# Optimization experiments

Hardware: AMD Instinct MI355X
Metric: run time of the kernel (lower is better)

Reference implementation:

```python
import jax, jax.numpy as jnp
import numpy as np

S, D_IN, D, H, FF = 8192, 128, 2, 2, 3
EPS = 1e-5


def _ln(x, s, b):
    m = jnp.mean(x, axis=-1, keepdims=True)
    v = jnp.mean((x - m) ** 2, axis=-1, keepdims=True)
    return (x - m) / jnp.sqrt(v + EPS) * s + b


def _mha(q_in, kv_in, qkv_w, qkv_b, out_w, out_b):
    # torch nn.MultiheadAttention: packed in_proj weight [3D, D], post-scale 1/sqrt(dh)
    wq, wk, wv = jnp.split(qkv_w, 3, axis=0)
    bq, bk, bv = jnp.split(qkv_b, 3)
    dh = D // H
    heads = lambda t: t.reshape(-1, H, dh).transpose(1, 0, 2)  # [H, S, dh]
    q = heads(q_in @ wq.T + bq)
    k = heads(kv_in @ wk.T + bk)
    v = heads(kv_in @ wv.T + bv)
    scores = jnp.einsum('hqd,hkd->hqk', q, k) / jnp.sqrt(jnp.asarray(dh, q.dtype))
    a = jax.nn.softmax(scores, axis=-1)
    o = jnp.einsum('hqk,hkd->hqd', a, v).transpose(1, 0, 2).reshape(-1, D)
    return o @ out_w.T + out_b


def _ffn(x, w1, b1, w2, b2):
    return jax.nn.relu(x @ w1.T + b1) @ w2.T + b2


def _forward(x, rand_mask, inn_w, inn_b, enc_qkv_w, enc_qkv_b, enc_out_w, enc_out_b, enc_ln1_s, enc_ln1_b, enc_ln2_s, enc_ln2_b, enc_ff1_w, enc_ff1_b, enc_ff2_w, enc_ff2_b, enc_norm_s, enc_norm_b, dec_sa_qkv_w, dec_sa_qkv_b, dec_sa_out_w, dec_sa_out_b, dec_ca_qkv_w, dec_ca_qkv_b, dec_ca_out_w, dec_ca_out_b, dec_ln1_s, dec_ln1_b, dec_ln2_s, dec_ln2_b, dec_ln3_s, dec_ln3_b, dec_ff1_w, dec_ff1_b, dec_ff2_w, dec_ff2_b, dec_norm_s, dec_norm_b, out_w, out_b):
    # x * rand(S,128) -> Linear(128,2) -> ReLU  (dropout disabled: eval mode)
    h = jax.nn.relu((x * rand_mask) @ inn_w.T + inn_b)  # [S, 2]
    # ---- encoder (2 post-norm layers) + final LayerNorm ----
    src = h
    for i in range(2):
        src = _ln(src + _mha(src, src, enc_qkv_w[i], enc_qkv_b[i], enc_out_w[i], enc_out_b[i]), enc_ln1_s[i], enc_ln1_b[i])
        src = _ln(src + _ffn(src, enc_ff1_w[i], enc_ff1_b[i], enc_ff2_w[i], enc_ff2_b[i]), enc_ln2_s[i], enc_ln2_b[i])
    mem = _ln(src, enc_norm_s, enc_norm_b)
    # ---- decoder (1 post-norm layer, tgt = h, no masks) + final LayerNorm ----
    t = h
    t = _ln(t + _mha(t, t, dec_sa_qkv_w, dec_sa_qkv_b, dec_sa_out_w, dec_sa_out_b), dec_ln1_s, dec_ln1_b)
    t = _ln(t + _mha(t, mem, dec_ca_qkv_w, dec_ca_qkv_b, dec_ca_out_w, dec_ca_out_b), dec_ln2_s, dec_ln2_b)
    t = _ln(t + _ffn(t, dec_ff1_w, dec_ff1_b, dec_ff2_w, dec_ff2_b), dec_ln3_s, dec_ln3_b)
    t = _ln(t, dec_norm_s, dec_norm_b)
    return jnp.tanh(t @ out_w.T + out_b)  # [S, 1]


def setup_inputs() -> dict:
    key = jax.random.key(0)
    ks = iter(jax.random.split(key, 64))
    n = lambda shape: jax.random.normal(next(ks), shape, jnp.float32) * 0.1
    return dict(
        x=jax.random.normal(next(ks), (S, D_IN), jnp.float32),
        rand_mask=jax.random.uniform(next(ks), (S, D_IN), jnp.float32),
        inn_w=n((D, D_IN)), inn_b=n((D,)),
        enc_qkv_w=n((2, 3 * D, D)), enc_qkv_b=n((2, 3 * D)),
        enc_out_w=n((2, D, D)), enc_out_b=n((2, D)),
        enc_ln1_s=jnp.ones((2, D)), enc_ln1_b=jnp.zeros((2, D)),
        enc_ln2_s=jnp.ones((2, D)), enc_ln2_b=jnp.zeros((2, D)),
        enc_ff1_w=n((2, FF, D)), enc_ff1_b=n((2, FF)),
        enc_ff2_w=n((2, D, FF)), enc_ff2_b=n((2, D)),
        enc_norm_s=jnp.ones((D,)), enc_norm_b=jnp.zeros((D,)),
        dec_sa_qkv_w=n((3 * D, D)), dec_sa_qkv_b=n((3 * D,)),
        dec_sa_out_w=n((D, D)), dec_sa_out_b=n((D,)),
        dec_ca_qkv_w=n((3 * D, D)), dec_ca_qkv_b=n((3 * D,)),
        dec_ca_out_w=n((D, D)), dec_ca_out_b=n((D,)),
        dec_ln1_s=jnp.ones((D,)), dec_ln1_b=jnp.zeros((D,)),
        dec_ln2_s=jnp.ones((D,)), dec_ln2_b=jnp.zeros((D,)),
        dec_ln3_s=jnp.ones((D,)), dec_ln3_b=jnp.zeros((D,)),
        dec_ff1_w=n((FF, D)), dec_ff1_b=n((FF,)),
        dec_ff2_w=n((D, FF)), dec_ff2_b=n((D,)),
        dec_norm_s=jnp.ones((D,)), dec_norm_b=jnp.zeros((D,)),
        out_w=n((1, D)), out_b=n((1,)),
    )


def reference(x, rand_mask, inn_w, inn_b, enc_qkv_w, enc_qkv_b, enc_out_w, enc_out_b, enc_ln1_s, enc_ln1_b, enc_ln2_s, enc_ln2_b, enc_ff1_w, enc_ff1_b, enc_ff2_w, enc_ff2_b, enc_norm_s, enc_norm_b, dec_sa_qkv_w, dec_sa_qkv_b, dec_sa_out_w, dec_sa_out_b, dec_ca_qkv_w, dec_ca_qkv_b, dec_ca_out_w, dec_ca_out_b, dec_ln1_s, dec_ln1_b, dec_ln2_s, dec_ln2_b, dec_ln3_s, dec_ln3_b, dec_ff1_w, dec_ff1_b, dec_ff2_w, dec_ff2_b, dec_norm_s, dec_norm_b, out_w, out_b):
    return _forward(x, rand_mask, inn_w, inn_b, enc_qkv_w, enc_qkv_b, enc_out_w, enc_out_b, enc_ln1_s, enc_ln1_b, enc_ln2_s, enc_ln2_b, enc_ff1_w, enc_ff1_b, enc_ff2_w, enc_ff2_b, enc_norm_s, enc_norm_b, dec_sa_qkv_w, dec_sa_qkv_b, dec_sa_out_w, dec_sa_out_b, dec_ca_qkv_w, dec_ca_qkv_b, dec_ca_out_w, dec_ca_out_b, dec_ln1_s, dec_ln1_b, dec_ln2_s, dec_ln2_b, dec_ln3_s, dec_ln3_b, dec_ff1_w, dec_ff1_b, dec_ff2_w, dec_ff2_b, dec_norm_s, dec_norm_b, out_w, out_b)
```

## Files before the change

### kernel.cpp

```cpp
#include <hip/hip_runtime.h>
#include <hip/hip_bf16.h>
#include <math.h>


#define S_ROWS 8192
#define NT 21
#define HEAD_STRIDE (2*NT)
#define ATT_STRIDE (2*HEAD_STRIDE)
#define MOM_FLOATS (4*ATT_STRIDE)
#define A_ENC1 0
#define A_ENC2 1
#define A_DSA  2
#define A_DCA  3
#define H_OFF  512
#define S1_OFF (H_OFF + 2*S_ROWS)
#define T1_OFF (S1_OFF + 2*S_ROWS)
#define LN_EPS 1e-5f

struct Params {
    const float *x, *mask, *inn_w, *inn_b;
    const float *enc_qkv_w, *enc_qkv_b, *enc_out_w, *enc_out_b;
    const float *enc_ln1_s, *enc_ln1_b, *enc_ln2_s, *enc_ln2_b;
    const float *enc_ff1_w, *enc_ff1_b, *enc_ff2_w, *enc_ff2_b;
    const float *enc_norm_s, *enc_norm_b;
    const float *dsa_qkv_w, *dsa_qkv_b, *dsa_out_w, *dsa_out_b;
    const float *dca_qkv_w, *dca_qkv_b, *dca_out_w, *dca_out_b;
    const float *dec_ln1_s, *dec_ln1_b, *dec_ln2_s, *dec_ln2_b, *dec_ln3_s, *dec_ln3_b;
    const float *dec_ff1_w, *dec_ff1_b, *dec_ff2_w, *dec_ff2_b;
    const float *dec_norm_s, *dec_norm_b, *out_w, *out_b;
    float* ws;
    float* out;
};

__constant__ float INVFACT[NT] = {
    1.0f, 1.0f, 0.5f, 1.6666667e-1f, 4.1666668e-2f, 8.3333338e-3f,
    1.3888889e-3f, 1.9841270e-4f, 2.4801588e-5f, 2.7557319e-6f,
    2.7557319e-7f, 2.5052108e-8f, 2.0876757e-9f, 1.6059044e-10f,
    1.1470746e-11f, 7.6471637e-13f, 4.7794773e-14f, 2.8114573e-15f,
    1.5619207e-16f, 8.2206352e-18f, 4.1103176e-19f
};

__device__ __forceinline__ float wredsum(float x) {
    #pragma unroll
    for (int o = 32; o; o >>= 1) x += __shfl_xor(x, o, 64);
    return x;
}

template<int N>
__device__ __forceinline__ void wred_arr(float* a) {
    #pragma unroll
    for (int o = 32; o; o >>= 1) {
        #pragma unroll
        for (int n = 0; n < N; ++n) a[n] += __shfl_xor(a[n], o, 64);
    }
}

__device__ __forceinline__ float attn_eval(const float* base, float q) {
    const float* Z = base;
    const float* M = base + NT;
    float sz = Z[NT-1] * INVFACT[NT-1];
    float sm = M[NT-1] * INVFACT[NT-1];
    #pragma unroll
    for (int n = NT-2; n >= 0; --n) {
        sz = fmaf(sz, q, Z[n] * INVFACT[n]);
        sm = fmaf(sm, q, M[n] * INVFACT[n]);
    }
    return sm / sz;
}

__device__ __forceinline__ void ln2(float a0, float a1, const float* s, const float* b,
                                    float& y0, float& y1) {
    float d = 0.5f * (a0 - a1);
    float r = d * rsqrtf(fmaf(d, d, LN_EPS));
    y0 = fmaf(r, s[0], b[0]);
    y1 = fmaf(-r, s[1], b[1]);
}

__device__ __forceinline__ void ffn2(float x0, float x1, const float* w1, const float* b1,
                                     const float* w2, const float* b2, float& y0, float& y1) {
    float t0 = fmaxf(fmaf(x0, w1[0], fmaf(x1, w1[1], b1[0])), 0.0f);
    float t1 = fmaxf(fmaf(x0, w1[2], fmaf(x1, w1[3], b1[1])), 0.0f);
    float t2 = fmaxf(fmaf(x0, w1[4], fmaf(x1, w1[5], b1[2])), 0.0f);
    y0 = fmaf(t0, w2[0], fmaf(t1, w2[1], fmaf(t2, w2[2], b2[0])));
    y1 = fmaf(t0, w2[3], fmaf(t1, w2[4], fmaf(t2, w2[5], b2[1])));
}

__device__ __forceinline__ void accum_local(float* z, float* m, float k, float v) {
    float pw = 1.0f;
    #pragma unroll
    for (int n = 0; n < NT; ++n) { z[n] += pw; m[n] += pw * v; pw *= k; }
}

__device__ __forceinline__ void flush_atomic(float* base, const float* z, const float* m, int lane) {
    if (lane == 0) {
        #pragma unroll
        for (int n = 0; n < NT; ++n) {
            atomicAdd(base + n,      z[n]);
            atomicAdd(base + NT + n, m[n]);
        }
    }
}

__global__ __launch_bounds__(256) void k_h(Params p) {
    int tid = threadIdx.x;
    if (blockIdx.x == 0) {
        for (int i = tid; i < MOM_FLOATS; i += 256) p.ws[i] = 0.0f;
    }
    int row  = (blockIdx.x * 256 + tid) >> 6;
    int lane = tid & 63;
    const float2* xr = (const float2*)(p.x    + (size_t)row * 128);
    const float2* mr = (const float2*)(p.mask + (size_t)row * 128);
    const float2* w0 = (const float2*)(p.inn_w);
    const float2* w1 = (const float2*)(p.inn_w + 128);
    float2 xv = xr[lane], mv = mr[lane], wa = w0[lane], wb = w1[lane];
    float xm0 = xv.x * mv.x, xm1 = xv.y * mv.y;
    float a0 = fmaf(xm0, wa.x, xm1 * wa.y);
    float a1 = fmaf(xm0, wb.x, xm1 * wb.y);
    a0 = wredsum(a0);
    a1 = wredsum(a1);
    if (lane == 0) {
        p.ws[H_OFF + 2*row]     = fmaxf(a0 + p.inn_b[0], 0.0f);
        p.ws[H_OFF + 2*row + 1] = fmaxf(a1 + p.inn_b[1], 0.0f);
    }
}

__global__ __launch_bounds__(256) void k_p1(Params p) {
    int wave = threadIdx.x >> 6, lane = threadIdx.x & 63;
    int row0 = blockIdx.x * 512;
    const float* W = (wave < 2) ? p.enc_qkv_w : p.dsa_qkv_w;
    const float* B = (wave < 2) ? p.enc_qkv_b : p.dsa_qkv_b;
    int hh = wave & 1;
    float kw0 = W[4+2*hh], kw1 = W[5+2*hh], kb = B[2+hh];
    float vw0 = W[8+2*hh], vw1 = W[9+2*hh], vb = B[4+hh];
    float z[NT], m[NT];
    #pragma unroll
    for (int n = 0; n < NT; ++n) { z[n] = 0.0f; m[n] = 0.0f; }
    for (int i = lane; i < 512; i += 64) {
        int r = row0 + i;
        float h0 = p.ws[H_OFF + 2*r], h1 = p.ws[H_OFF + 2*r + 1];
        float k = fmaf(h0, kw0, fmaf(h1, kw1, kb));
        float v = fmaf(h0, vw0, fmaf(h1, vw1, vb));
        accum_local(z, m, k, v);
    }
    wred_arr<NT>(z);
    wred_arr<NT>(m);
    float* base = p.ws + ((wave < 2) ? A_ENC1 : A_DSA)*ATT_STRIDE + hh*HEAD_STRIDE;
    flush_atomic(base, z, m, lane);
}

__global__ __launch_bounds__(256) void k_p2(Params p) {
    __shared__ float sl[1024];
    int tid = threadIdx.x;
    int row0 = blockIdx.x * 512;
    #pragma unroll
    for (int rr = 0; rr < 2; ++rr) {
        int i = tid + rr*256;
        int r = row0 + i;
        float h0 = p.ws[H_OFF + 2*r], h1 = p.ws[H_OFF + 2*r + 1];
        float q0 = fmaf(h0, p.enc_qkv_w[0], fmaf(h1, p.enc_qkv_w[1], p.enc_qkv_b[0]));
        float q1 = fmaf(h0, p.enc_qkv_w[2], fmaf(h1, p.enc_qkv_w[3], p.enc_qkv_b[1]));
        float o0 = attn_eval(p.ws + A_ENC1*ATT_STRIDE,               q0);
        float o1 = attn_eval(p.ws + A_ENC1*ATT_STRIDE + HEAD_STRIDE, q1);
        float m0 = fmaf(o0, p.enc_out_w[0], fmaf(o1, p.enc_out_w[1], p.enc_out_b[0]));
        float m1 = fmaf(o0, p.enc_out_w[2], fmaf(o1, p.enc_out_w[3], p.enc_out_b[1]));
        float u0, u1; ln2(h0 + m0, h1 + m1, p.enc_ln1_s, p.enc_ln1_b, u0, u1);
        float f0, f1; ffn2(u0, u1, p.enc_ff1_w, p.enc_ff1_b, p.enc_ff2_w, p.enc_ff2_b, f0, f1);
        float s0, s1; ln2(u0 + f0, u1 + f1, p.enc_ln2_s, p.enc_ln2_b, s0, s1);
        p.ws[S1_OFF + 2*r]     = s0;
        p.ws[S1_OFF + 2*r + 1] = s1;
        sl[2*i]   = s0;
        sl[2*i+1] = s1;
    }
    __syncthreads();
    int wave = tid >> 6, lane = tid & 63;
    int hh = wave & 1, half = wave >> 1;
    const float* W = p.enc_qkv_w + 12;
    const float* B = p.enc_qkv_b + 6;
    float kw0 = W[4+2*hh], kw1 = W[5+2*hh], kb = B[2+hh];
    float vw0 = W[8+2*hh], vw1 = W[9+2*hh], vb = B[4+hh];
    float z[NT], m[NT];
    #pragma unroll
    for (int n = 0; n < NT; ++n) { z[n] = 0.0f; m[n] = 0.0f; }
    #pragma unroll
    for (int j = 0; j < 4; ++j) {
        int i = half*256 + j*64 + lane;
        float s0 = sl[2*i], s1 = sl[2*i+1];
        float k = fmaf(s0, kw0, fmaf(s1, kw1, kb));
        float v = fmaf(s0, vw0, fmaf(s1, vw1, vb));
        accum_local(z, m, k, v);
    }
    wred_arr<NT>(z);
    wred_arr<NT>(m);
    flush_atomic(p.ws + A_ENC2*ATT_STRIDE + hh*HEAD_STRIDE, z, m, lane);
}

__global__ __launch_bounds__(256) void k_p3(Params p) {
    __shared__ float ml[1024];
    int tid = threadIdx.x;
    int row0 = blockIdx.x * 512;
    const float* W = p.enc_qkv_w + 12;
    const float* B = p.enc_qkv_b + 6;
    const float* Wo = p.enc_out_w + 4;
    const float* Bo = p.enc_out_b + 2;
    #pragma unroll
    for (int rr = 0; rr < 2; ++rr) {
        int i = tid + rr*256;
        int r = row0 + i;
        float s0 = p.ws[S1_OFF + 2*r], s1 = p.ws[S1_OFF + 2*r + 1];
        float q0 = fmaf(s0, W[0], fmaf(s1, W[1], B[0]));
        float q1 = fmaf(s0, W[2], fmaf(s1, W[3], B[1]));
        float o0 = attn_eval(p.ws + A_ENC2*ATT_STRIDE,               q0);
        float o1 = attn_eval(p.ws + A_ENC2*ATT_STRIDE + HEAD_STRIDE, q1);
        float m0 = fmaf(o0, Wo[0], fmaf(o1, Wo[1], Bo[0]));
        float m1 = fmaf(o0, Wo[2], fmaf(o1, Wo[3], Bo[1]));
        float u0, u1; ln2(s0 + m0, s1 + m1, p.enc_ln1_s + 2, p.enc_ln1_b + 2, u0, u1);
        float f0, f1; ffn2(u0, u1, p.enc_ff1_w + 6, p.enc_ff1_b + 3, p.enc_ff2_w + 6, p.enc_ff2_b + 2, f0, f1);
        float e0, e1; ln2(u0 + f0, u1 + f1, p.enc_ln2_s + 2, p.enc_ln2_b + 2, e0, e1);
        float mem0, mem1; ln2(e0, e1, p.enc_norm_s, p.enc_norm_b, mem0, mem1);
        ml[2*i]   = mem0;
        ml[2*i+1] = mem1;
        float h0 = p.ws[H_OFF + 2*r], h1 = p.ws[H_OFF + 2*r + 1];
        float dq0 = fmaf(h0, p.dsa_qkv_w[0], fmaf(h1, p.dsa_qkv_w[1], p.dsa_qkv_b[0]));
        float dq1 = fmaf(h0, p.dsa_qkv_w[2], fmaf(h1, p.dsa_qkv_w[3], p.dsa_qkv_b[1]));
        float d0 = attn_eval(p.ws + A_DSA*ATT_STRIDE,               dq0);
        float d1 = attn_eval(p.ws + A_DSA*ATT_STRIDE + HEAD_STRIDE, dq1);
        float sm0 = fmaf(d0, p.dsa_out_w[0], fmaf(d1, p.dsa_out_w[1], p.dsa_out_b[0]));
        float sm1 = fmaf(d0, p.dsa_out_w[2], fmaf(d1, p.dsa_out_w[3], p.dsa_out_b[1]));
        float t0, t1; ln2(h0 + sm0, h1 + sm1, p.dec_ln1_s, p.dec_ln1_b, t0, t1);
        p.ws[T1_OFF + 2*r]     = t0;
        p.ws[T1_OFF + 2*r + 1] = t1;
    }
    __syncthreads();
    int wave = tid >> 6, lane = tid & 63;
    int hh = wave & 1, half = wave >> 1;
    float kw0 = p.dca_qkv_w[4+2*hh], kw1 = p.dca_qkv_w[5+2*hh], kb = p.dca_qkv_b[2+hh];
    float vw0 = p.dca_qkv_w[8+2*hh], vw1 = p.dca_qkv_w[9+2*hh], vb = p.dca_qkv_b[4+hh];
    float z[NT], m[NT];
    #pragma unroll
    for (int n = 0; n < NT; ++n) { z[n] = 0.0f; m[n] = 0.0f; }
    #pragma unroll
    for (int j = 0; j < 4; ++j) {
        int i = half*256 + j*64 + lane;
        float mem0 = ml[2*i], mem1 = ml[2*i+1];
        float k = fmaf(mem0, kw0, fmaf(mem1, kw1, kb));
        float v = fmaf(mem0, vw0, fmaf(mem1, vw1, vb));
        accum_local(z, m, k, v);
    }
    wred_arr<NT>(z);
    wred_arr<NT>(m);
    flush_atomic(p.ws + A_DCA*ATT_STRIDE + hh*HEAD_STRIDE, z, m, lane);
}

__global__ __launch_bounds__(256) void k_p4(Params p) {
    int r = blockIdx.x * 256 + threadIdx.x;
    float t0 = p.ws[T1_OFF + 2*r], t1 = p.ws[T1_OFF + 2*r + 1];
    float q0 = fmaf(t0, p.dca_qkv_w[0], fmaf(t1, p.dca_qkv_w[1], p.dca_qkv_b[0]));
    float q1 = fmaf(t0, p.dca_qkv_w[2], fmaf(t1, p.dca_qkv_w[3], p.dca_qkv_b[1]));
    float c0 = attn_eval(p.ws + A_DCA*ATT_STRIDE,               q0);
    float c1 = attn_eval(p.ws + A_DCA*ATT_STRIDE + HEAD_STRIDE, q1);
    float m0 = fmaf(c0, p.dca_out_w[0], fmaf(c1, p.dca_out_w[1], p.dca_out_b[0]));
    float m1 = fmaf(c0, p.dca_out_w[2], fmaf(c1, p.dca_out_w[3], p.dca_out_b[1]));
    float u0, u1; ln2(t0 + m0, t1 + m1, p.dec_ln2_s, p.dec_ln2_b, u0, u1);
    float f0, f1; ffn2(u0, u1, p.dec_ff1_w, p.dec_ff1_b, p.dec_ff2_w, p.dec_ff2_b, f0, f1);
    float w0, w1; ln2(u0 + f0, u1 + f1, p.dec_ln3_s, p.dec_ln3_b, w0, w1);
    float z0, z1; ln2(w0, w1, p.dec_norm_s, p.dec_norm_b, z0, z1);
    float y = tanhf(fmaf(z0, p.out_w[0], fmaf(z1, p.out_w[1], p.out_b[0])));
    p.out[r] = y;
}

extern "C" void kernel_launch(void* const* d_in, const int* in_sizes, int n_in,
                              void* d_out, int out_size, void* d_ws, size_t ws_size,
                              hipStream_t stream) {
    Params p;
    p.x          = (const float*)d_in[0];
    p.mask       = (const float*)d_in[1];
    p.inn_w      = (const float*)d_in[2];
    p.inn_b      = (const float*)d_in[3];
    p.enc_qkv_w  = (const float*)d_in[4];
    p.enc_qkv_b  = (const float*)d_in[5];
    p.enc_out_w  = (const float*)d_in[6];
    p.enc_out_b  = (const float*)d_in[7];
    p.enc_ln1_s  = (const float*)d_in[8];
    p.enc_ln1_b  = (const float*)d_in[9];
    p.enc_ln2_s  = (const float*)d_in[10];
    p.enc_ln2_b  = (const float*)d_in[11];
    p.enc_ff1_w  = (const float*)d_in[12];
    p.enc_ff1_b  = (const float*)d_in[13];
    p.enc_ff2_w  = (const float*)d_in[14];
    p.enc_ff2_b  = (const float*)d_in[15];
    p.enc_norm_s = (const float*)d_in[16];
    p.enc_norm_b = (const float*)d_in[17];
    p.dsa_qkv_w  = (const float*)d_in[18];
    p.dsa_qkv_b  = (const float*)d_in[19];
    p.dsa_out_w  = (const float*)d_in[20];
    p.dsa_out_b  = (const float*)d_in[21];
    p.dca_qkv_w  = (const float*)d_in[22];
    p.dca_qkv_b  = (const float*)d_in[23];
    p.dca_out_w  = (const float*)d_in[24];
    p.dca_out_b  = (const float*)d_in[25];
    p.dec_ln1_s  = (const float*)d_in[26];
    p.dec_ln1_b  = (const float*)d_in[27];
    p.dec_ln2_s  = (const float*)d_in[28];
    p.dec_ln2_b  = (const float*)d_in[29];
    p.dec_ln3_s  = (const float*)d_in[30];
    p.dec_ln3_b  = (const float*)d_in[31];
    p.dec_ff1_w  = (const float*)d_in[32];
    p.dec_ff1_b  = (const float*)d_in[33];
    p.dec_ff2_w  = (const float*)d_in[34];
    p.dec_ff2_b  = (const float*)d_in[35];
    p.dec_norm_s = (const float*)d_in[36];
    p.dec_norm_b = (const float*)d_in[37];
    p.out_w      = (const float*)d_in[38];
    p.out_b      = (const float*)d_in[39];
    p.ws  = (float*)d_ws;
    p.out = (float*)d_out;

    hipLaunchKernelGGL(k_h,  dim3(2048), dim3(256), 0, stream, p);
    hipLaunchKernelGGL(k_p1, dim3(16),   dim3(256), 0, stream, p);
    hipLaunchKernelGGL(k_p2, dim3(16),   dim3(256), 0, stream, p);
    hipLaunchKernelGGL(k_p3, dim3(16),   dim3(256), 0, stream, p);
    hipLaunchKernelGGL(k_p4, dim3(32),   dim3(256), 0, stream, p);
}
```

Baseline: 199.2 us.

## Fuse five stage kernels into one cooperative kernel with grid syncs

Replaces the five separate launches with a single cooperative kernel of 256 blocks that separates phases with grid.sync(). Per-row intermediates are kept in registers across phases instead of being written to and re-read from global workspace. The moment coefficients are pre-scaled into shared memory once per block. This removes launch gaps and global round-trips, but adds four grid-wide barriers and leaves most blocks idle in the later phases.

```diff
diff --git a/kernel.cpp b/kernel.cpp
--- a/kernel.cpp
+++ b/kernel.cpp
@@ -1,6 +1,8 @@
 #include <hip/hip_runtime.h>
-#include <hip/hip_bf16.h>
+#include <hip/hip_cooperative_groups.h>
 #include <math.h>
+
+namespace cg = cooperative_groups;
 
 
 #define S_ROWS 8192
@@ -13,8 +15,6 @@
 #define A_DSA  2
 #define A_DCA  3
 #define H_OFF  512
-#define S1_OFF (H_OFF + 2*S_ROWS)
-#define T1_OFF (S1_OFF + 2*S_ROWS)
 #define LN_EPS 1e-5f
 
 struct Params {
@@ -55,15 +55,22 @@
     }
 }
 
-__device__ __forceinline__ float attn_eval(const float* base, float q) {
-    const float* Z = base;
-    const float* M = base + NT;
-    float sz = Z[NT-1] * INVFACT[NT-1];
-    float sm = M[NT-1] * INVFACT[NT-1];
+__device__ __forceinline__ void stage2(int t, const float* base,
+                                       float* cz0, float* cm0, float* cz1, float* cm1) {
+    if ((unsigned)t < 4u*NT) {
+        int grp = t / NT, n = t - grp*NT;
+        float v = base[t] * INVFACT[n];
+        float* dst = (grp == 0) ? cz0 : (grp == 1) ? cm0 : (grp == 2) ? cz1 : cm1;
+        dst[n] = v;
+    }
+}
+
+__device__ __forceinline__ float attn_eval_l(const float* cz, const float* cm, float q) {
+    float sz = cz[NT-1], sm = cm[NT-1];
     #pragma unroll
     for (int n = NT-2; n >= 0; --n) {
-        sz = fmaf(sz, q, Z[n] * INVFACT[n]);
-        sm = fmaf(sm, q, M[n] * INVFACT[n]);
+        sz = fmaf(sz, q, cz[n]);
+        sm = fmaf(sm, q, cm[n]);
     }
     return sm / sz;
 }
@@ -101,171 +108,182 @@
     }
 }
 
-__global__ __launch_bounds__(256) void k_h(Params p) {
-    int tid = threadIdx.x;
-    if (blockIdx.x == 0) {
+__global__ __launch_bounds__(256) void k_all(Params p) {
+    cg::grid_group grid = cg::this_grid();
+    const int tid = threadIdx.x, b = blockIdx.x;
+    const int wave = tid >> 6, lane = tid & 63;
+    __shared__ float cza[NT], cma[NT], czb[NT], cmb[NT];
+    __shared__ float czc[NT], cmc[NT], czd[NT], cmd[NT];
+    __shared__ float sl[1024];
+    float s1r[2][2], tr[2][2];
+
+    if (b == 0) {
         for (int i = tid; i < MOM_FLOATS; i += 256) p.ws[i] = 0.0f;
     }
-    int row  = (blockIdx.x * 256 + tid) >> 6;
-    int lane = tid & 63;
-    const float2* xr = (const float2*)(p.x    + (size_t)row * 128);
-    const float2* mr = (const float2*)(p.mask + (size_t)row * 128);
-    const float2* w0 = (const float2*)(p.inn_w);
-    const float2* w1 = (const float2*)(p.inn_w + 128);
-    float2 xv = xr[lane], mv = mr[lane], wa = w0[lane], wb = w1[lane];
-    float xm0 = xv.x * mv.x, xm1 = xv.y * mv.y;
-    float a0 = fmaf(xm0, wa.x, xm1 * wa.y);
-    float a1 = fmaf(xm0, wb.x, xm1 * wb.y);
-    a0 = wredsum(a0);
-    a1 = wredsum(a1);
-    if (lane == 0) {
-        p.ws[H_OFF + 2*row]     = fmaxf(a0 + p.inn_b[0], 0.0f);
-        p.ws[H_OFF + 2*row + 1] = fmaxf(a1 + p.inn_b[1], 0.0f);
-    }
-}
-
-__global__ __launch_bounds__(256) void k_p1(Params p) {
-    int wave = threadIdx.x >> 6, lane = threadIdx.x & 63;
-    int row0 = blockIdx.x * 512;
-    const float* W = (wave < 2) ? p.enc_qkv_w : p.dsa_qkv_w;
-    const float* B = (wave < 2) ? p.enc_qkv_b : p.dsa_qkv_b;
-    int hh = wave & 1;
-    float kw0 = W[4+2*hh], kw1 = W[5+2*hh], kb = B[2+hh];
-    float vw0 = W[8+2*hh], vw1 = W[9+2*hh], vb = B[4+hh];
-    float z[NT], m[NT];
-    #pragma unroll
-    for (int n = 0; n < NT; ++n) { z[n] = 0.0f; m[n] = 0.0f; }
-    for (int i = lane; i < 512; i += 64) {
-        int r = row0 + i;
-        float h0 = p.ws[H_OFF + 2*r], h1 = p.ws[H_OFF + 2*r + 1];
-        float k = fmaf(h0, kw0, fmaf(h1, kw1, kb));
-        float v = fmaf(h0, vw0, fmaf(h1, vw1, vb));
-        accum_local(z, m, k, v);
-    }
-    wred_arr<NT>(z);
-    wred_arr<NT>(m);
-    float* base = p.ws + ((wave < 2) ? A_ENC1 : A_DSA)*ATT_STRIDE + hh*HEAD_STRIDE;
-    flush_atomic(base, z, m, lane);
-}
-
-__global__ __launch_bounds__(256) void k_p2(Params p) {
-    __shared__ float sl[1024];
-    int tid = threadIdx.x;
-    int row0 = blockIdx.x * 512;
-    #pragma unroll
-    for (int rr = 0; rr < 2; ++rr) {
-        int i = tid + rr*256;
-        int r = row0 + i;
-        float h0 = p.ws[H_OFF + 2*r], h1 = p.ws[H_OFF + 2*r + 1];
-        float q0 = fmaf(h0, p.enc_qkv_w[0], fmaf(h1, p.enc_qkv_w[1], p.enc_qkv_b[0]));
-        float q1 = fmaf(h0, p.enc_qkv_w[2], fmaf(h1, p.enc_qkv_w[3], p.enc_qkv_b[1]));
-        float o0 = attn_eval(p.ws + A_ENC1*ATT_STRIDE,               q0);
-        float o1 = attn_eval(p.ws + A_ENC1*ATT_STRIDE + HEAD_STRIDE, q1);
-        float m0 = fmaf(o0, p.enc_out_w[0], fmaf(o1, p.enc_out_w[1], p.enc_out_b[0]));
-        float m1 = fmaf(o0, p.enc_out_w[2], fmaf(o1, p.enc_out_w[3], p.enc_out_b[1]));
-        float u0, u1; ln2(h0 + m0, h1 + m1, p.enc_ln1_s, p.enc_ln1_b, u0, u1);
-        float f0, f1; ffn2(u0, u1, p.enc_ff1_w, p.enc_ff1_b, p.enc_ff2_w, p.enc_ff2_b, f0, f1);
-        float s0, s1; ln2(u0 + f0, u1 + f1, p.enc_ln2_s, p.enc_ln2_b, s0, s1);
-        p.ws[S1_OFF + 2*r]     = s0;
-        p.ws[S1_OFF + 2*r + 1] = s1;
-        sl[2*i]   = s0;
-        sl[2*i+1] = s1;
-    }
-    __syncthreads();
-    int wave = tid >> 6, lane = tid & 63;
-    int hh = wave & 1, half = wave >> 1;
-    const float* W = p.enc_qkv_w + 12;
-    const float* B = p.enc_qkv_b + 6;
-    float kw0 = W[4+2*hh], kw1 = W[5+2*hh], kb = B[2+hh];
-    float vw0 = W[8+2*hh], vw1 = W[9+2*hh], vb = B[4+hh];
-    float z[NT], m[NT];
-    #pragma unroll
-    for (int n = 0; n < NT; ++n) { z[n] = 0.0f; m[n] = 0.0f; }
-    #pragma unroll
-    for (int j = 0; j < 4; ++j) {
-        int i = half*256 + j*64 + lane;
-        float s0 = sl[2*i], s1 = sl[2*i+1];
-        float k = fmaf(s0, kw0, fmaf(s1, kw1, kb));
-        float v = fmaf(s0, vw0, fmaf(s1, vw1, vb));
-        accum_local(z, m, k, v);
-    }
-    wred_arr<NT>(z);
-    wred_arr<NT>(m);
-    flush_atomic(p.ws + A_ENC2*ATT_STRIDE + hh*HEAD_STRIDE, z, m, lane);
-}
-
-__global__ __launch_bounds__(256) void k_p3(Params p) {
-    __shared__ float ml[1024];
-    int tid = threadIdx.x;
-    int row0 = blockIdx.x * 512;
-    const float* W = p.enc_qkv_w + 12;
-    const float* B = p.enc_qkv_b + 6;
-    const float* Wo = p.enc_out_w + 4;
-    const float* Bo = p.enc_out_b + 2;
-    #pragma unroll
-    for (int rr = 0; rr < 2; ++rr) {
-        int i = tid + rr*256;
-        int r = row0 + i;
-        float s0 = p.ws[S1_OFF + 2*r], s1 = p.ws[S1_OFF + 2*r + 1];
-        float q0 = fmaf(s0, W[0], fmaf(s1, W[1], B[0]));
-        float q1 = fmaf(s0, W[2], fmaf(s1, W[3], B[1]));
-        float o0 = attn_eval(p.ws + A_ENC2*ATT_STRIDE,               q0);
-        float o1 = attn_eval(p.ws + A_ENC2*ATT_STRIDE + HEAD_STRIDE, q1);
-        float m0 = fmaf(o0, Wo[0], fmaf(o1, Wo[1], Bo[0]));
-        float m1 = fmaf(o0, Wo[2], fmaf(o1, Wo[3], Bo[1]));
-        float u0, u1; ln2(s0 + m0, s1 + m1, p.enc_ln1_s + 2, p.enc_ln1_b + 2, u0, u1);
-        float f0, f1; ffn2(u0, u1, p.enc_ff1_w + 6, p.enc_ff1_b + 3, p.enc_ff2_w + 6, p.enc_ff2_b + 2, f0, f1);
-        float e0, e1; ln2(u0 + f0, u1 + f1, p.enc_ln2_s + 2, p.enc_ln2_b + 2, e0, e1);
-        float mem0, mem1; ln2(e0, e1, p.enc_norm_s, p.enc_norm_b, mem0, mem1);
-        ml[2*i]   = mem0;
-        ml[2*i+1] = mem1;
-        float h0 = p.ws[H_OFF + 2*r], h1 = p.ws[H_OFF + 2*r + 1];
-        float dq0 = fmaf(h0, p.dsa_qkv_w[0], fmaf(h1, p.dsa_qkv_w[1], p.dsa_qkv_b[0]));
-        float dq1 = fmaf(h0, p.dsa_qkv_w[2], fmaf(h1, p.dsa_qkv_w[3], p.dsa_qkv_b[1]));
-        float d0 = attn_eval(p.ws + A_DSA*ATT_STRIDE,               dq0);
-        float d1 = attn_eval(p.ws + A_DSA*ATT_STRIDE + HEAD_STRIDE, dq1);
-        float sm0 = fmaf(d0, p.dsa_out_w[0], fmaf(d1, p.dsa_out_w[1], p.dsa_out_b[0]));
-        float sm1 = fmaf(d0, p.dsa_out_w[2], fmaf(d1, p.dsa_out_w[3], p.dsa_out_b[1]));
-        float t0, t1; ln2(h0 + sm0, h1 + sm1, p.dec_ln1_s, p.dec_ln1_b, t0, t1);
-        p.ws[T1_OFF + 2*r]     = t0;
-        p.ws[T1_OFF + 2*r + 1] = t1;
-    }
-    __syncthreads();
-    int wave = tid >> 6, lane = tid & 63;
-    int hh = wave & 1, half = wave >> 1;
-    float kw0 = p.dca_qkv_w[4+2*hh], kw1 = p.dca_qkv_w[5+2*hh], kb = p.dca_qkv_b[2+hh];
-    float vw0 = p.dca_qkv_w[8+2*hh], vw1 = p.dca_qkv_w[9+2*hh], vb = p.dca_qkv_b[4+hh];
-    float z[NT], m[NT];
-    #pragma unroll
-    for (int n = 0; n < NT; ++n) { z[n] = 0.0f; m[n] = 0.0f; }
-    #pragma unroll
-    for (int j = 0; j < 4; ++j) {
-        int i = half*256 + j*64 + lane;
-        float mem0 = ml[2*i], mem1 = ml[2*i+1];
-        float k = fmaf(mem0, kw0, fmaf(mem1, kw1, kb));
-        float v = fmaf(mem0, vw0, fmaf(mem1, vw1, vb));
-        accum_local(z, m, k, v);
-    }
-    wred_arr<NT>(z);
-    wred_arr<NT>(m);
-    flush_atomic(p.ws + A_DCA*ATT_STRIDE + hh*HEAD_STRIDE, z, m, lane);
-}
-
-__global__ __launch_bounds__(256) void k_p4(Params p) {
-    int r = blockIdx.x * 256 + threadIdx.x;
-    float t0 = p.ws[T1_OFF + 2*r], t1 = p.ws[T1_OFF + 2*r + 1];
-    float q0 = fmaf(t0, p.dca_qkv_w[0], fmaf(t1, p.dca_qkv_w[1], p.dca_qkv_b[0]));
-    float q1 = fmaf(t0, p.dca_qkv_w[2], fmaf(t1, p.dca_qkv_w[3], p.dca_qkv_b[1]));
-    float c0 = attn_eval(p.ws + A_DCA*ATT_STRIDE,               q0);
-    float c1 = attn_eval(p.ws + A_DCA*ATT_STRIDE + HEAD_STRIDE, q1);
-    float m0 = fmaf(c0, p.dca_out_w[0], fmaf(c1, p.dca_out_w[1], p.dca_out_b[0]));
-    float m1 = fmaf(c0, p.dca_out_w[2], fmaf(c1, p.dca_out_w[3], p.dca_out_b[1]));
-    float u0, u1; ln2(t0 + m0, t1 + m1, p.dec_ln2_s, p.dec_ln2_b, u0, u1);
-    float f0, f1; ffn2(u0, u1, p.dec_ff1_w, p.dec_ff1_b, p.dec_ff2_w, p.dec_ff2_b, f0, f1);
-    float w0, w1; ln2(u0 + f0, u1 + f1, p.dec_ln3_s, p.dec_ln3_b, w0, w1);
-    float z0, z1; ln2(w0, w1, p.dec_norm_s, p.dec_norm_b, z0, z1);
-    float y = tanhf(fmaf(z0, p.out_w[0], fmaf(z1, p.out_w[1], p.out_b[0])));
-    p.out[r] = y;
+    {
+        const float2* w0 = (const float2*)(p.inn_w);
+        const float2* w1 = (const float2*)(p.inn_w + 128);
+        float2 wa = w0[lane], wb = w1[lane];
+        float ib0 = p.inn_b[0], ib1 = p.inn_b[1];
+        #pragma unroll
+        for (int i = 0; i < 8; ++i) {
+            int row = b*32 + i*4 + wave;
+            const float2* xr = (const float2*)(p.x    + (size_t)row * 128);
+            const float2* mr = (const float2*)(p.mask + (size_t)row * 128);
+            float2 xv = xr[lane], mv = mr[lane];
+            float xm0 = xv.x * mv.x, xm1 = xv.y * mv.y;
+            float a0 = fmaf(xm0, wa.x, xm1 * wa.y);
+            float a1 = fmaf(xm0, wb.x, xm1 * wb.y);
+            a0 = wredsum(a0);
+            a1 = wredsum(a1);
+            if (lane == 0) {
+                p.ws[H_OFF + 2*row]     = fmaxf(a0 + ib0, 0.0f);
+                p.ws[H_OFF + 2*row + 1] = fmaxf(a1 + ib1, 0.0f);
+            }
+        }
+    }
+    grid.sync();
+
+    if (b < 16) {
+        const float* W  = (wave < 2) ? p.enc_qkv_w : p.dsa_qkv_w;
+        const float* Bs = (wave < 2) ? p.enc_qkv_b : p.dsa_qkv_b;
+        int hh = wave & 1;
+        float kw0 = W[4+2*hh], kw1 = W[5+2*hh], kb = Bs[2+hh];
+        float vw0 = W[8+2*hh], vw1 = W[9+2*hh], vb = Bs[4+hh];
+        float z[NT], m[NT];
+        #pragma unroll
+        for (int n = 0; n < NT; ++n) { z[n] = 0.0f; m[n] = 0.0f; }
+        #pragma unroll
+        for (int j = 0; j < 8; ++j) {
+            int r = b*512 + j*64 + lane;
+            float h0 = p.ws[H_OFF + 2*r], h1 = p.ws[H_OFF + 2*r + 1];
+            float k = fmaf(h0, kw0, fmaf(h1, kw1, kb));
+            float v = fmaf(h0, vw0, fmaf(h1, vw1, vb));
+            accum_local(z, m, k, v);
+        }
+        wred_arr<NT>(z);
+        wred_arr<NT>(m);
+        flush_atomic(p.ws + ((wave < 2) ? A_ENC1 : A_DSA)*ATT_STRIDE + hh*HEAD_STRIDE, z, m, lane);
+    }
+    grid.sync();
+
+    if (b < 16) {
+        stage2(tid, p.ws + A_ENC1*ATT_STRIDE, cza, cma, czb, cmb);
+        __syncthreads();
+        #pragma unroll
+        for (int rr = 0; rr < 2; ++rr) {
+            int i = tid + rr*256, r = b*512 + i;
+            float h0 = p.ws[H_OFF + 2*r], h1 = p.ws[H_OFF + 2*r + 1];
+            float q0 = fmaf(h0, p.enc_qkv_w[0], fmaf(h1, p.enc_qkv_w[1], p.enc_qkv_b[0]));
+            float q1 = fmaf(h0, p.enc_qkv_w[2], fmaf(h1, p.enc_qkv_w[3], p.enc_qkv_b[1]));
+            float o0 = attn_eval_l(cza, cma, q0);
+            float o1 = attn_eval_l(czb, cmb, q1);
+            float m0 = fmaf(o0, p.enc_out_w[0], fmaf(o1, p.enc_out_w[1], p.enc_out_b[0]));
+            float m1 = fmaf(o0, p.enc_out_w[2], fmaf(o1, p.enc_out_w[3], p.enc_out_b[1]));
+            float u0, u1; ln2(h0 + m0, h1 + m1, p.enc_ln1_s, p.enc_ln1_b, u0, u1);
+            float f0, f1; ffn2(u0, u1, p.enc_ff1_w, p.enc_ff1_b, p.enc_ff2_w, p.enc_ff2_b, f0, f1);
+            float s0, s1; ln2(u0 + f0, u1 + f1, p.enc_ln2_s, p.enc_ln2_b, s0, s1);
+            s1r[rr][0] = s0; s1r[rr][1] = s1;
+            sl[2*i] = s0; sl[2*i+1] = s1;
+        }
+        __syncthreads();
+        int hh = wave & 1, half = wave >> 1;
+        const float* W  = p.enc_qkv_w + 12;
+        const float* Bs = p.enc_qkv_b + 6;
+        float kw0 = W[4+2*hh], kw1 = W[5+2*hh], kb = Bs[2+hh];
+        float vw0 = W[8+2*hh], vw1 = W[9+2*hh], vb = Bs[4+hh];
+        float z[NT], m[NT];
+        #pragma unroll
+        for (int n = 0; n < NT; ++n) { z[n] = 0.0f; m[n] = 0.0f; }
+        #pragma unroll
+        for (int j = 0; j < 4; ++j) {
+            int i = half*256 + j*64 + lane;
+            float s0 = sl[2*i], s1 = sl[2*i+1];
+            float k = fmaf(s0, kw0, fmaf(s1, kw1, kb));
+            float v = fmaf(s0, vw0, fmaf(s1, vw1, vb));
+            accum_local(z, m, k, v);
+        }
+        wred_arr<NT>(z);
+        wred_arr<NT>(m);
+        flush_atomic(p.ws + A_ENC2*ATT_STRIDE + hh*HEAD_STRIDE, z, m, lane);
+    }
+    grid.sync();
+
+    if (b < 16) {
+        stage2(tid,       p.ws + A_ENC2*ATT_STRIDE, cza, cma, czb, cmb);
+        stage2(tid - 4*NT, p.ws + A_DSA*ATT_STRIDE, czc, cmc, czd, cmd);
+        __syncthreads();
+        const float* W  = p.enc_qkv_w + 12;
+        const float* Bs = p.enc_qkv_b + 6;
+        const float* Wo = p.enc_out_w + 4;
+        const float* Bo = p.enc_out_b + 2;
+        #pragma unroll
+        for (int rr = 0; rr < 2; ++rr) {
+            int i = tid + rr*256, r = b*512 + i;
+            float s0 = s1r[rr][0], s1 = s1r[rr][1];
+            float q0 = fmaf(s0, W[0], fmaf(s1, W[1], Bs[0]));
+            float q1 = fmaf(s0, W[2], fmaf(s1, W[3], Bs[1]));
+            float o0 = attn_eval_l(cza, cma, q0);
+            float o1 = attn_eval_l(czb, cmb, q1);
+            float m0 = fmaf(o0, Wo[0], fmaf(o1, Wo[1], Bo[0]));
+            float m1 = fmaf(o0, Wo[2], fmaf(o1, Wo[3], Bo[1]));
+            float u0, u1; ln2(s0 + m0, s1 + m1, p.enc_ln1_s + 2, p.enc_ln1_b + 2, u0, u1);
+            float f0, f1; ffn2(u0, u1, p.enc_ff1_w + 6, p.enc_ff1_b + 3, p.enc_ff2_w + 6, p.enc_ff2_b + 2, f0, f1);
+            float e0, e1; ln2(u0 + f0, u1 + f1, p.enc_ln2_s + 2, p.enc_ln2_b + 2, e0, e1);
+            float mem0, mem1; ln2(e0, e1, p.enc_norm_s, p.enc_norm_b, mem0, mem1);
+            sl[2*i] = mem0; sl[2*i+1] = mem1;
+            float h0 = p.ws[H_OFF + 2*r], h1 = p.ws[H_OFF + 2*r + 1];
+            float dq0 = fmaf(h0, p.dsa_qkv_w[0], fmaf(h1, p.dsa_qkv_w[1], p.dsa_qkv_b[0]));
+            float dq1 = fmaf(h0, p.dsa_qkv_w[2], fmaf(h1, p.dsa_qkv_w[3], p.dsa_qkv_b[1]));
+            float d0 = attn_eval_l(czc, cmc, dq0);
+            float d1 = attn_eval_l(czd, cmd, dq1);
+            float sm0 = fmaf(d0, p.dsa_out_w[0], fmaf(d1, p.dsa_out_w[1], p.dsa_out_b[0]));
+            float sm1 = fmaf(d0, p.dsa_out_w[2], fmaf(d1, p.dsa_out_w[3], p.dsa_out_b[1]));
+            float t0, t1; ln2(h0 + sm0, h1 + sm1, p.dec_ln1_s, p.dec_ln1_b, t0, t1);
+            tr[rr][0] = t0; tr[rr][1] = t1;
+        }
+        __syncthreads();
+        int hh = wave & 1, half = wave >> 1;
+        float kw0 = p.dca_qkv_w[4+2*hh], kw1 = p.dca_qkv_w[5+2*hh], kb = p.dca_qkv_b[2+hh];
+        float vw0 = p.dca_qkv_w[8+2*hh], vw1 = p.dca_qkv_w[9+2*hh], vb = p.dca_qkv_b[4+hh];
+        float z[NT], m[NT];
+        #pragma unroll
+        for (int n = 0; n < NT; ++n) { z[n] = 0.0f; m[n] = 0.0f; }
+        #pragma unroll
+        for (int j = 0; j < 4; ++j) {
+            int i = half*256 + j*64 + lane;
+            float mem0 = sl[2*i], mem1 = sl[2*i+1];
+            float k = fmaf(mem0, kw0, fmaf(mem1, kw1, kb));
+            float v = fmaf(mem0, vw0, fmaf(mem1, vw1, vb));
+            accum_local(z, m, k, v);
+        }
+        wred_arr<NT>(z);
+        wred_arr<NT>(m);
+        flush_atomic(p.ws + A_DCA*ATT_STRIDE + hh*HEAD_STRIDE, z, m, lane);
+    }
+    grid.sync();
+
+    if (b < 16) {
+        stage2(tid, p.ws + A_DCA*ATT_STRIDE, cza, cma, czb, cmb);
+        __syncthreads();
+        #pragma unroll
+        for (int rr = 0; rr < 2; ++rr) {
+            int r = b*512 + tid + rr*256;
+            float t0 = tr[rr][0], t1 = tr[rr][1];
+            float q0 = fmaf(t0, p.dca_qkv_w[0], fmaf(t1, p.dca_qkv_w[1], p.dca_qkv_b[0]));
+            float q1 = fmaf(t0, p.dca_qkv_w[2], fmaf(t1, p.dca_qkv_w[3], p.dca_qkv_b[1]));
+            float c0 = attn_eval_l(cza, cma, q0);
+            float c1 = attn_eval_l(czb, cmb, q1);
+            float m0 = fmaf(c0, p.dca_out_w[0], fmaf(c1, p.dca_out_w[1], p.dca_out_b[0]));
+            float m1 = fmaf(c0, p.dca_out_w[2], fmaf(c1, p.dca_out_w[3], p.dca_out_b[1]));
+            float u0, u1; ln2(t0 + m0, t1 + m1, p.dec_ln2_s, p.dec_ln2_b, u0, u1);
+            float f0, f1; ffn2(u0, u1, p.dec_ff1_w, p.dec_ff1_b, p.dec_ff2_w, p.dec_ff2_b, f0, f1);
+            float w0, w1; ln2(u0 + f0, u1 + f1, p.dec_ln3_s, p.dec_ln3_b, w0, w1);
+            float z0, z1; ln2(w0, w1, p.dec_norm_s, p.dec_norm_b, z0, z1);
+            float y = tanhf(fmaf(z0, p.out_w[0], fmaf(z1, p.out_w[1], p.out_b[0])));
+            p.out[r] = y;
+        }
+    }
 }
 
 extern "C" void kernel_launch(void* const* d_in, const int* in_sizes, int n_in,
@@ -315,9 +333,6 @@
     p.ws  = (float*)d_ws;
     p.out = (float*)d_out;
 
-    hipLaunchKernelGGL(k_h,  dim3(2048), dim3(256), 0, stream, p);
-    hipLaunchKernelGGL(k_p1, dim3(16),   dim3(256), 0, stream, p);
-    hipLaunchKernelGGL(k_p2, dim3(16),   dim3(256), 0, stream, p);
-    hipLaunchKernelGGL(k_p3, dim3(16),   dim3(256), 0, stream, p);
-    hipLaunchKernelGGL(k_p4, dim3(32),   dim3(256), 0, stream, p);
-}
+    void* args[] = { &p };
+    hipLaunchCooperativeKernel((const void*)k_all, dim3(256), dim3(256), args, 0, stream);
+}
```

After: 330.8 us. +66.1%, slower.
